# Kernel optimization log

Measured on AMD Instinct MI355X. Metric: run time of the kernel, lower is better.

## Reference

```python
import jax, jax.numpy as jnp
import numpy as np

D_MODEL = 64  # head dim; temper = sqrt(d_model)
B, TQ, TK, D = 64, 2048, 2048, 64


def setup_inputs() -> dict:
    key = jax.random.key(0)
    kq, kk, kv, km = jax.random.split(key, 4)
    q = jax.random.normal(kq, (B, TQ, D), dtype=jnp.float32)
    k = jax.random.normal(kk, (B, TK, D), dtype=jnp.float32)
    v = jax.random.normal(kv, (B, TK, D), dtype=jnp.float32)
    # boolean mask, True = masked out (matches torch masked_fill semantics)
    attn_mask = jax.random.randint(km, (B, TQ, TK), 0, 2) == 1
    return {"q": q, "k": k, "v": v, "attn_mask": attn_mask}


def reference(q, k, v, attn_mask):
    temper = float(D_MODEL) ** 0.5
    # attn = bmm(q, k^T) / temper  -> [B, TQ, TK]
    attn = jnp.einsum("bqd,bkd->bqk", q, k) / temper
    attn = jnp.where(attn_mask, jnp.float32(-1e18), attn)
    # BottleSoftmax(dim=1) flattens [B,TQ,TK]->[B*TQ,TK] then softmax(dim=1),
    # i.e., softmax over the key axis.
    attn = jax.nn.softmax(attn, axis=-1)
    # dropout omitted (eval / deterministic reference)
    out = jnp.einsum("bqk,bkd->bqd", attn, v)
    return (out, attn)
```

## Files before the change

### kernel.cpp

```cpp
#include <hip/hip_runtime.h>
#include <hip/hip_bf16.h>

#define BATCHES 64
#define T 2048
#define DHEAD 64
#define QT 64
#define KTILE 64
#define NKT (T / KTILE)

typedef __bf16 bf16x8 __attribute__((ext_vector_type(8)));
typedef float f32x4 __attribute__((ext_vector_type(4)));

__device__ __forceinline__ unsigned short f2bf(float x) {
  union { float f; unsigned u; } v; v.f = x;
  unsigned r = v.u + 0x7FFFu + ((v.u >> 16) & 1u);
  return (unsigned short)(r >> 16);
}

__device__ __forceinline__ void stage64x64(const float* __restrict__ src,
                                           unsigned short* dst, int tid) {
  const float4* s4 = (const float4*)src;
#pragma unroll
  for (int s = 0; s < 4; ++s) {
    int i4 = tid + s * 256;
    float4 val = s4[i4];
    unsigned lo = f2bf(val.x) | ((unsigned)f2bf(val.y) << 16);
    unsigned hi = f2bf(val.z) | ((unsigned)f2bf(val.w) << 16);
    *(uint2*)(dst + i4 * 4) = make_uint2(lo, hi);
  }
}

__global__ __launch_bounds__(256, 4)
void sdpa_kernel(const float* __restrict__ q, const float* __restrict__ kk,
                 const float* __restrict__ vv, const int* __restrict__ mask,
                 float* __restrict__ out, float* __restrict__ attn) {
  __shared__ __attribute__((aligned(16))) unsigned short Qs[QT * DHEAD];
  __shared__ __attribute__((aligned(16))) unsigned short Ks[KTILE * DHEAD];
  __shared__ __attribute__((aligned(16))) unsigned short VT[DHEAD * 72];
  __shared__ __attribute__((aligned(16))) unsigned short Ps[QT * 72];

  const int tid  = threadIdx.x;
  const int w    = tid >> 6;
  const int lane = tid & 63;
  const int quad = lane >> 4;
  const int l15  = lane & 15;

  const int batch = blockIdx.x >> 5;
  const int q0    = (blockIdx.x & 31) * QT;

  stage64x64(q + ((size_t)batch * T + q0) * DHEAD, Qs, tid);
  __syncthreads();

  bf16x8 qf0 = *(const bf16x8*)(Qs + (w * 16 + l15) * DHEAD + quad * 8);
  bf16x8 qf1 = *(const bf16x8*)(Qs + (w * 16 + l15) * DHEAD + 32 + quad * 8);

  f32x4 oacc[4];
#pragma unroll
  for (int nt = 0; nt < 4; ++nt) oacc[nt] = (f32x4){0.f, 0.f, 0.f, 0.f};
  float lp[4] = {0.f, 0.f, 0.f, 0.f};

  for (int kt = 0; kt < NKT; ++kt) {
    __syncthreads();
    stage64x64(kk + ((size_t)batch * T + kt * KTILE) * DHEAD, Ks, tid);
    {
      const float4* s4 = (const float4*)(vv + ((size_t)batch * T + kt * KTILE) * DHEAD);
#pragma unroll
      for (int s = 0; s < 4; ++s) {
        int i4 = tid + s * 256;
        float4 val = s4[i4];
        int c  = i4 >> 4;
        int dd = (i4 & 15) * 4;
        VT[(dd + 0) * 72 + c] = f2bf(val.x);
        VT[(dd + 1) * 72 + c] = f2bf(val.y);
        VT[(dd + 2) * 72 + c] = f2bf(val.z);
        VT[(dd + 3) * 72 + c] = f2bf(val.w);
      }
    }
    __syncthreads();

#pragma unroll
    for (int ct = 0; ct < 4; ++ct) {
      bf16x8 kf0 = *(const bf16x8*)(Ks + (ct * 16 + l15) * DHEAD + quad * 8);
      bf16x8 kf1 = *(const bf16x8*)(Ks + (ct * 16 + l15) * DHEAD + 32 + quad * 8);
      f32x4 acc = (f32x4){0.f, 0.f, 0.f, 0.f};
      acc = __builtin_amdgcn_mfma_f32_16x16x32_bf16(qf0, kf0, acc, 0, 0, 0);
      acc = __builtin_amdgcn_mfma_f32_16x16x32_bf16(qf1, kf1, acc, 0, 0, 0);
      const int col = kt * KTILE + ct * 16 + l15;
      const size_t idx0 = ((size_t)batch * T + (q0 + w * 16 + quad * 4)) * T + col;
#pragma unroll
      for (int reg = 0; reg < 4; ++reg) {
        int m = mask[idx0 + (size_t)reg * T];
        float s = fminf(acc[reg] * 0.125f, 60.f);
        float e = m ? 0.f : __expf(s);
        lp[reg] += e;
        Ps[(w * 16 + quad * 4 + reg) * 72 + ct * 16 + l15] = f2bf(e);
      }
    }
    __syncthreads();

    bf16x8 pa0 = *(const bf16x8*)(Ps + (w * 16 + l15) * 72 + quad * 8);
    bf16x8 pa1 = *(const bf16x8*)(Ps + (w * 16 + l15) * 72 + 32 + quad * 8);
#pragma unroll
    for (int nt = 0; nt < 4; ++nt) {
      bf16x8 vb0 = *(const bf16x8*)(VT + (nt * 16 + l15) * 72 + quad * 8);
      bf16x8 vb1 = *(const bf16x8*)(VT + (nt * 16 + l15) * 72 + 32 + quad * 8);
      oacc[nt] = __builtin_amdgcn_mfma_f32_16x16x32_bf16(pa0, vb0, oacc[nt], 0, 0, 0);
      oacc[nt] = __builtin_amdgcn_mfma_f32_16x16x32_bf16(pa1, vb1, oacc[nt], 0, 0, 0);
    }
  }

  float rinv[4];
#pragma unroll
  for (int reg = 0; reg < 4; ++reg) {
    float x = lp[reg];
    x += __shfl_xor(x, 1);
    x += __shfl_xor(x, 2);
    x += __shfl_xor(x, 4);
    x += __shfl_xor(x, 8);
    rinv[reg] = x > 0.f ? 1.0f / x : 0.f;
  }

#pragma unroll
  for (int nt = 0; nt < 4; ++nt) {
#pragma unroll
    for (int reg = 0; reg < 4; ++reg) {
      int row = q0 + w * 16 + quad * 4 + reg;
      out[((size_t)batch * T + row) * DHEAD + nt * 16 + l15] = oacc[nt][reg] * rinv[reg];
    }
  }

  for (int kt = NKT - 1; kt >= 0; --kt) {
    __syncthreads();
    stage64x64(kk + ((size_t)batch * T + kt * KTILE) * DHEAD, Ks, tid);
    __syncthreads();
#pragma unroll
    for (int ct = 0; ct < 4; ++ct) {
      bf16x8 kf0 = *(const bf16x8*)(Ks + (ct * 16 + l15) * DHEAD + quad * 8);
      bf16x8 kf1 = *(const bf16x8*)(Ks + (ct * 16 + l15) * DHEAD + 32 + quad * 8);
      f32x4 acc = (f32x4){0.f, 0.f, 0.f, 0.f};
      acc = __builtin_amdgcn_mfma_f32_16x16x32_bf16(qf0, kf0, acc, 0, 0, 0);
      acc = __builtin_amdgcn_mfma_f32_16x16x32_bf16(qf1, kf1, acc, 0, 0, 0);
      const int col = kt * KTILE + ct * 16 + l15;
      const size_t idx0 = ((size_t)batch * T + (q0 + w * 16 + quad * 4)) * T + col;
#pragma unroll
      for (int reg = 0; reg < 4; ++reg) {
        int m = mask[idx0 + (size_t)reg * T];
        float s = fminf(acc[reg] * 0.125f, 60.f);
        float p = m ? 0.f : __expf(s) * rinv[reg];
        attn[idx0 + (size_t)reg * T] = p;
      }
    }
  }
}

extern "C" void kernel_launch(void* const* d_in, const int* in_sizes, int n_in,
                              void* d_out, int out_size, void* d_ws, size_t ws_size,
                              hipStream_t stream) {
  const float* q    = (const float*)d_in[0];
  const float* k    = (const float*)d_in[1];
  const float* v    = (const float*)d_in[2];
  const int*   mask = (const int*)d_in[3];
  float* out  = (float*)d_out;
  float* attn = out + (size_t)BATCHES * T * DHEAD;

  dim3 grid(BATCHES * (T / QT));
  sdpa_kernel<<<grid, 256, 0, stream>>>(q, k, v, mask, out, attn);
}
```

Measured before the change: 2.109 ms.

## Precompute bf16 K/V^T and keep the full probability row block in LDS

Adds a pre-pass kernel that converts K to bf16 and V to transposed bf16 in workspace. The main kernel uses 32-row query blocks with 8 waves, computes all exp scores once into a swizzled 128KB LDS buffer, and reuses them for both P·V and the normalized attn write. This removes the second QK^T pass and the second read of the mask. The kernel also uses vectorized nontemporal mask loads and stores and a remapped block order. The large LDS footprint limits occupancy, and attn is now written from bf16-rounded probabilities, which loses some precision.

```diff
diff --git a/kernel.cpp b/kernel.cpp
--- a/kernel.cpp
+++ b/kernel.cpp
@@ -1,43 +1,67 @@
 #include <hip/hip_runtime.h>
-#include <hip/hip_bf16.h>
 
 #define BATCHES 64
 #define T 2048
 #define DHEAD 64
-#define QT 64
-#define KTILE 64
-#define NKT (T / KTILE)
+#define QT 32
+#define NW 8
 
 typedef __bf16 bf16x8 __attribute__((ext_vector_type(8)));
 typedef float f32x4 __attribute__((ext_vector_type(4)));
+typedef int   i32x4 __attribute__((ext_vector_type(4)));
+typedef float fltx4 __attribute__((ext_vector_type(4)));
 
-__device__ __forceinline__ unsigned short f2bf(float x) {
+static __device__ __forceinline__ unsigned short f2bf(float x) {
   union { float f; unsigned u; } v; v.f = x;
   unsigned r = v.u + 0x7FFFu + ((v.u >> 16) & 1u);
   return (unsigned short)(r >> 16);
 }
+static __device__ __forceinline__ float bf2f(unsigned s) {
+  union { unsigned u; float f; } v; v.u = s << 16; return v.f;
+}
 
-__device__ __forceinline__ void stage64x64(const float* __restrict__ src,
-                                           unsigned short* dst, int tid) {
-  const float4* s4 = (const float4*)src;
+__global__ __launch_bounds__(256)
+void pre_convert(const float* __restrict__ kk, const float* __restrict__ vv,
+                 unsigned short* __restrict__ Kbf, unsigned short* __restrict__ VTbf) {
+  const int bid = blockIdx.x;
+  if (bid < 4096) {
+    const size_t i8 = (size_t)bid * 256 + threadIdx.x;
+    const float4* s4 = (const float4*)kk + i8 * 2;
+    const float4 a = s4[0], b = s4[1];
+    uint4 r;
+    r.x = f2bf(a.x) | ((unsigned)f2bf(a.y) << 16);
+    r.y = f2bf(a.z) | ((unsigned)f2bf(a.w) << 16);
+    r.z = f2bf(b.x) | ((unsigned)f2bf(b.y) << 16);
+    r.w = f2bf(b.z) | ((unsigned)f2bf(b.w) << 16);
+    *(uint4*)(Kbf + i8 * 8) = r;
+  } else {
+    const int b2 = bid - 4096;
+    const int batch = b2 >> 5;
+    const int k0 = (b2 & 31) * 64;
 #pragma unroll
-  for (int s = 0; s < 4; ++s) {
-    int i4 = tid + s * 256;
-    float4 val = s4[i4];
-    unsigned lo = f2bf(val.x) | ((unsigned)f2bf(val.y) << 16);
-    unsigned hi = f2bf(val.z) | ((unsigned)f2bf(val.w) << 16);
-    *(uint2*)(dst + i4 * 4) = make_uint2(lo, hi);
+    for (int uu = 0; uu < 2; ++uu) {
+      const int u = (int)threadIdx.x + uu * 256;
+      const int d = u >> 3;
+      const int seg = (u & 7) * 8;
+      const float* src = vv + ((size_t)batch * T + k0 + seg) * DHEAD + d;
+      uint4 r;
+      r.x = f2bf(src[0 * DHEAD]) | ((unsigned)f2bf(src[1 * DHEAD]) << 16);
+      r.y = f2bf(src[2 * DHEAD]) | ((unsigned)f2bf(src[3 * DHEAD]) << 16);
+      r.z = f2bf(src[4 * DHEAD]) | ((unsigned)f2bf(src[5 * DHEAD]) << 16);
+      r.w = f2bf(src[6 * DHEAD]) | ((unsigned)f2bf(src[7 * DHEAD]) << 16);
+      *(uint4*)(VTbf + ((size_t)batch * DHEAD + d) * T + k0 + seg) = r;
+    }
   }
 }
 
-__global__ __launch_bounds__(256, 4)
-void sdpa_kernel(const float* __restrict__ q, const float* __restrict__ kk,
-                 const float* __restrict__ vv, const int* __restrict__ mask,
-                 float* __restrict__ out, float* __restrict__ attn) {
-  __shared__ __attribute__((aligned(16))) unsigned short Qs[QT * DHEAD];
-  __shared__ __attribute__((aligned(16))) unsigned short Ks[KTILE * DHEAD];
-  __shared__ __attribute__((aligned(16))) unsigned short VT[DHEAD * 72];
-  __shared__ __attribute__((aligned(16))) unsigned short Ps[QT * 72];
+__global__ __launch_bounds__(512, 2)
+void sdpa_main(const float* __restrict__ q, const int* __restrict__ mask,
+               const unsigned short* __restrict__ Kbf,
+               const unsigned short* __restrict__ VTbf,
+               float* __restrict__ out, float* __restrict__ attn) {
+  __shared__ __attribute__((aligned(16))) unsigned short Ps[QT * T];
+  __shared__ float l_part[QT][NW];
+  __shared__ float rinv_s[QT];
 
   const int tid  = threadIdx.x;
   const int w    = tid >> 6;
@@ -45,110 +69,112 @@
   const int quad = lane >> 4;
   const int l15  = lane & 15;
 
-  const int batch = blockIdx.x >> 5;
-  const int q0    = (blockIdx.x & 31) * QT;
+  int bid = blockIdx.x;
+  bid = ((bid & 7) << 9) | (bid >> 3);
+  const int batch = bid >> 6;
+  const int q0    = (bid & 63) * QT;
 
-  stage64x64(q + ((size_t)batch * T + q0) * DHEAD, Qs, tid);
-  __syncthreads();
-
-  bf16x8 qf0 = *(const bf16x8*)(Qs + (w * 16 + l15) * DHEAD + quad * 8);
-  bf16x8 qf1 = *(const bf16x8*)(Qs + (w * 16 + l15) * DHEAD + 32 + quad * 8);
-
-  f32x4 oacc[4];
+  bf16x8 qf[2][2];
 #pragma unroll
-  for (int nt = 0; nt < 4; ++nt) oacc[nt] = (f32x4){0.f, 0.f, 0.f, 0.f};
-  float lp[4] = {0.f, 0.f, 0.f, 0.f};
-
-  for (int kt = 0; kt < NKT; ++kt) {
-    __syncthreads();
-    stage64x64(kk + ((size_t)batch * T + kt * KTILE) * DHEAD, Ks, tid);
-    {
-      const float4* s4 = (const float4*)(vv + ((size_t)batch * T + kt * KTILE) * DHEAD);
+  for (int rt = 0; rt < 2; ++rt) {
+    const float* qrow = q + ((size_t)batch * T + q0 + rt * 16 + l15) * DHEAD;
 #pragma unroll
-      for (int s = 0; s < 4; ++s) {
-        int i4 = tid + s * 256;
-        float4 val = s4[i4];
-        int c  = i4 >> 4;
-        int dd = (i4 & 15) * 4;
-        VT[(dd + 0) * 72 + c] = f2bf(val.x);
-        VT[(dd + 1) * 72 + c] = f2bf(val.y);
-        VT[(dd + 2) * 72 + c] = f2bf(val.z);
-        VT[(dd + 3) * 72 + c] = f2bf(val.w);
-      }
-    }
-    __syncthreads();
-
-#pragma unroll
-    for (int ct = 0; ct < 4; ++ct) {
-      bf16x8 kf0 = *(const bf16x8*)(Ks + (ct * 16 + l15) * DHEAD + quad * 8);
-      bf16x8 kf1 = *(const bf16x8*)(Ks + (ct * 16 + l15) * DHEAD + 32 + quad * 8);
-      f32x4 acc = (f32x4){0.f, 0.f, 0.f, 0.f};
-      acc = __builtin_amdgcn_mfma_f32_16x16x32_bf16(qf0, kf0, acc, 0, 0, 0);
-      acc = __builtin_amdgcn_mfma_f32_16x16x32_bf16(qf1, kf1, acc, 0, 0, 0);
-      const int col = kt * KTILE + ct * 16 + l15;
-      const size_t idx0 = ((size_t)batch * T + (q0 + w * 16 + quad * 4)) * T + col;
-#pragma unroll
-      for (int reg = 0; reg < 4; ++reg) {
-        int m = mask[idx0 + (size_t)reg * T];
-        float s = fminf(acc[reg] * 0.125f, 60.f);
-        float e = m ? 0.f : __expf(s);
-        lp[reg] += e;
-        Ps[(w * 16 + quad * 4 + reg) * 72 + ct * 16 + l15] = f2bf(e);
-      }
-    }
-    __syncthreads();
-
-    bf16x8 pa0 = *(const bf16x8*)(Ps + (w * 16 + l15) * 72 + quad * 8);
-    bf16x8 pa1 = *(const bf16x8*)(Ps + (w * 16 + l15) * 72 + 32 + quad * 8);
-#pragma unroll
-    for (int nt = 0; nt < 4; ++nt) {
-      bf16x8 vb0 = *(const bf16x8*)(VT + (nt * 16 + l15) * 72 + quad * 8);
-      bf16x8 vb1 = *(const bf16x8*)(VT + (nt * 16 + l15) * 72 + 32 + quad * 8);
-      oacc[nt] = __builtin_amdgcn_mfma_f32_16x16x32_bf16(pa0, vb0, oacc[nt], 0, 0, 0);
-      oacc[nt] = __builtin_amdgcn_mfma_f32_16x16x32_bf16(pa1, vb1, oacc[nt], 0, 0, 0);
+    for (int h = 0; h < 2; ++h) {
+      float4 a = *(const float4*)(qrow + h * 32 + quad * 8);
+      float4 b = *(const float4*)(qrow + h * 32 + quad * 8 + 4);
+      union { unsigned u[4]; bf16x8 v; } r;
+      r.u[0] = f2bf(a.x) | ((unsigned)f2bf(a.y) << 16);
+      r.u[1] = f2bf(a.z) | ((unsigned)f2bf(a.w) << 16);
+      r.u[2] = f2bf(b.x) | ((unsigned)f2bf(b.y) << 16);
+      r.u[3] = f2bf(b.z) | ((unsigned)f2bf(b.w) << 16);
+      qf[rt][h] = r.v;
     }
   }
 
-  float rinv[4];
+  float lp0 = 0.f, lp1 = 0.f;
+  const int kbase = w * (T / NW);
+#pragma unroll 4
+  for (int ct = 0; ct < 16; ++ct) {
+    const int key0 = kbase + ct * 16;
+    const unsigned short* krow =
+        Kbf + ((size_t)batch * T + key0 + l15) * DHEAD + quad * 8;
+    const bf16x8 kf0 = *(const bf16x8*)(krow);
+    const bf16x8 kf1 = *(const bf16x8*)(krow + 32);
+#pragma unroll
+    for (int rt = 0; rt < 2; ++rt) {
+      const int row = rt * 16 + l15;
+      const i32x4 m4 = __builtin_nontemporal_load(
+          (const i32x4*)(mask + ((size_t)batch * T + q0 + row) * T + key0 + quad * 4));
+      f32x4 acc = (f32x4){0.f, 0.f, 0.f, 0.f};
+      acc = __builtin_amdgcn_mfma_f32_16x16x32_bf16(kf0, qf[rt][0], acc, 0, 0, 0);
+      acc = __builtin_amdgcn_mfma_f32_16x16x32_bf16(kf1, qf[rt][1], acc, 0, 0, 0);
+      const float e0 = m4.x ? 0.f : __expf(fminf(acc[0] * 0.125f, 60.f));
+      const float e1 = m4.y ? 0.f : __expf(fminf(acc[1] * 0.125f, 60.f));
+      const float e2 = m4.z ? 0.f : __expf(fminf(acc[2] * 0.125f, 60.f));
+      const float e3 = m4.w ? 0.f : __expf(fminf(acc[3] * 0.125f, 60.f));
+      if (rt == 0) lp0 += (e0 + e1) + (e2 + e3);
+      else         lp1 += (e0 + e1) + (e2 + e3);
+      uint2 pk;
+      pk.x = f2bf(e0) | ((unsigned)f2bf(e1) << 16);
+      pk.y = f2bf(e2) | ((unsigned)f2bf(e3) << 16);
+      char* p = (char*)Ps + row * (T * 2) +
+                ((((key0 + quad * 4) * 2)) ^ ((row & 7) << 4));
+      *(uint2*)p = pk;
+    }
+  }
+  {
+    float x0 = lp0; x0 += __shfl_xor(x0, 16); x0 += __shfl_xor(x0, 32);
+    float x1 = lp1; x1 += __shfl_xor(x1, 16); x1 += __shfl_xor(x1, 32);
+    if (quad == 0) { l_part[l15][w] = x0; l_part[16 + l15][w] = x1; }
+  }
+  __syncthreads();
+
+  if (tid < QT) {
+    float s = 0.f;
+#pragma unroll
+    for (int j = 0; j < NW; ++j) s += l_part[tid][j];
+    rinv_s[tid] = s > 0.f ? 1.0f / s : 0.f;
+  }
+
+  const int rt = w >> 2, nt = w & 3;
+  const unsigned short* vrow =
+      VTbf + ((size_t)batch * DHEAD + nt * 16 + l15) * T + quad * 8;
+  const int prow = rt * 16 + l15;
+  const char* pbase = (const char*)Ps + prow * (T * 2);
+  const int sw = (prow & 7) << 4;
+  f32x4 o = (f32x4){0.f, 0.f, 0.f, 0.f};
+#pragma unroll 8
+  for (int ks = 0; ks < 64; ++ks) {
+    const bf16x8 pa = *(const bf16x8*)(pbase + ((ks * 64 + quad * 16) ^ sw));
+    const bf16x8 vb = *(const bf16x8*)(vrow + ks * 32);
+    o = __builtin_amdgcn_mfma_f32_16x16x32_bf16(pa, vb, o, 0, 0, 0);
+  }
+  __syncthreads();
+
 #pragma unroll
   for (int reg = 0; reg < 4; ++reg) {
-    float x = lp[reg];
-    x += __shfl_xor(x, 1);
-    x += __shfl_xor(x, 2);
-    x += __shfl_xor(x, 4);
-    x += __shfl_xor(x, 8);
-    rinv[reg] = x > 0.f ? 1.0f / x : 0.f;
+    const int row = rt * 16 + quad * 4 + reg;
+    out[((size_t)batch * T + q0 + row) * DHEAD + nt * 16 + l15] =
+        o[reg] * rinv_s[row];
   }
 
 #pragma unroll
-  for (int nt = 0; nt < 4; ++nt) {
+  for (int r = 0; r < 4; ++r) {
+    const int row = w * 4 + r;
+    const float rv = rinv_s[row];
+    const char* pr = (const char*)Ps + row * (T * 2);
+    const int swr = (row & 7) << 4;
+    float* arow = attn + ((size_t)batch * T + q0 + row) * T;
 #pragma unroll
-    for (int reg = 0; reg < 4; ++reg) {
-      int row = q0 + w * 16 + quad * 4 + reg;
-      out[((size_t)batch * T + row) * DHEAD + nt * 16 + l15] = oacc[nt][reg] * rinv[reg];
-    }
-  }
-
-  for (int kt = NKT - 1; kt >= 0; --kt) {
-    __syncthreads();
-    stage64x64(kk + ((size_t)batch * T + kt * KTILE) * DHEAD, Ks, tid);
-    __syncthreads();
-#pragma unroll
-    for (int ct = 0; ct < 4; ++ct) {
-      bf16x8 kf0 = *(const bf16x8*)(Ks + (ct * 16 + l15) * DHEAD + quad * 8);
-      bf16x8 kf1 = *(const bf16x8*)(Ks + (ct * 16 + l15) * DHEAD + 32 + quad * 8);
-      f32x4 acc = (f32x4){0.f, 0.f, 0.f, 0.f};
-      acc = __builtin_amdgcn_mfma_f32_16x16x32_bf16(qf0, kf0, acc, 0, 0, 0);
-      acc = __builtin_amdgcn_mfma_f32_16x16x32_bf16(qf1, kf1, acc, 0, 0, 0);
-      const int col = kt * KTILE + ct * 16 + l15;
-      const size_t idx0 = ((size_t)batch * T + (q0 + w * 16 + quad * 4)) * T + col;
-#pragma unroll
-      for (int reg = 0; reg < 4; ++reg) {
-        int m = mask[idx0 + (size_t)reg * T];
-        float s = fminf(acc[reg] * 0.125f, 60.f);
-        float p = m ? 0.f : __expf(s) * rinv[reg];
-        attn[idx0 + (size_t)reg * T] = p;
-      }
+    for (int seg = 0; seg < 8; ++seg) {
+      const int col = seg * 256 + lane * 4;
+      const uint2 pk = *(const uint2*)(pr + ((col * 2) ^ swr));
+      fltx4 o4;
+      o4.x = bf2f(pk.x & 0xffffu) * rv;
+      o4.y = bf2f(pk.x >> 16) * rv;
+      o4.z = bf2f(pk.y & 0xffffu) * rv;
+      o4.w = bf2f(pk.y >> 16) * rv;
+      __builtin_nontemporal_store(o4, (fltx4*)(arow + col));
     }
   }
 }
@@ -163,6 +189,9 @@
   float* out  = (float*)d_out;
   float* attn = out + (size_t)BATCHES * T * DHEAD;
 
-  dim3 grid(BATCHES * (T / QT));
-  sdpa_kernel<<<grid, 256, 0, stream>>>(q, k, v, mask, out, attn);
+  unsigned short* Kbf  = (unsigned short*)d_ws;
+  unsigned short* VTbf = Kbf + (size_t)BATCHES * T * DHEAD;
+
+  pre_convert<<<dim3(6144), dim3(256), 0, stream>>>(k, v, Kbf, VTbf);
+  sdpa_main<<<dim3(4096), dim3(512), 0, stream>>>(q, mask, Kbf, VTbf, out, attn);
 }
```

Measured after the change: 2.048 ms. 1.03x faster.
